# Optimization experiments

Measured on AMD Instinct MI355X. Metric: run time of the kernel, lower is better.

The kernel has to match this reference:

```python
import jax, jax.numpy as jnp
import numpy as np

NEG_SLOPE = 0.01  # torch nn.LeakyReLU default


def setup_inputs() -> dict:
    key = jax.random.key(0)
    k1, k2, k3, k4, k5 = jax.random.split(key, 5)
    B, C, N, O = 32, 512, 1024, 512
    x = jax.random.normal(k1, (B, C, N), dtype=jnp.float32)
    wq = jax.random.normal(k2, (C,), dtype=jnp.float32) * (1.0 / np.sqrt(C))
    wk = jax.random.normal(k3, (C,), dtype=jnp.float32) * (1.0 / np.sqrt(C))
    wm = jax.random.normal(k4, (O, C), dtype=jnp.float32) * (1.0 / np.sqrt(C))
    bm = jax.random.normal(k5, (O,), dtype=jnp.float32) * 0.01
    return {"x": x, "wq": wq, "wk": wk, "wm": wm, "bm": bm}


def reference(x, wq, wk, wm, bm):
    # x: [B, C, N]
    q = jnp.einsum('c,bcn->bn', wq, x)            # [B, N] (Conv1d C->1, k=1, no bias)
    k = jnp.einsum('c,bcn->bn', wk, x)            # [B, N]
    scores = q[:, None, :] + k[:, :, None]        # [B, N, N] additive broadcast
    scores = jnp.where(scores > 0, scores, NEG_SLOPE * scores)  # LeakyReLU
    att = jax.nn.softmax(scores, axis=-1)         # softmax over last dim
    agg = jnp.einsum('bcn,bmn->bcm', x, att)      # weighted aggregation [B, C, N]
    out = jnp.einsum('oc,bcm->bom', wm, agg) + bm[None, :, None]  # Conv1d k=1
    return jax.nn.relu(out)
```

## Files before the change

kernel.cpp:

```cpp
#include <hip/hip_runtime.h>


constexpr int B = 32, C = 512, N = 1024, O = 512;
constexpr float L2E = 1.4426950408889634f;

typedef _Float16 half8 __attribute__((ext_vector_type(8)));
typedef _Float16 half4v __attribute__((ext_vector_type(4)));
typedef _Float16 half2v __attribute__((ext_vector_type(2)));
typedef float f32x4 __attribute__((ext_vector_type(4)));

#if __has_builtin(__builtin_amdgcn_exp2f)
#define EXP2(x) __builtin_amdgcn_exp2f(x)
#else
#define EXP2(x) exp2f(x)
#endif

__device__ __forceinline__ half8 cvt8(float4 a, float4 b) {
  half8 h;
  h[0] = (_Float16)a.x; h[1] = (_Float16)a.y; h[2] = (_Float16)a.z; h[3] = (_Float16)a.w;
  h[4] = (_Float16)b.x; h[5] = (_Float16)b.y; h[6] = (_Float16)b.z; h[7] = (_Float16)b.w;
  return h;
}

__device__ __forceinline__ unsigned fenc(float x) {
  unsigned u = __float_as_uint(x);
  return (u & 0x80000000u) ? ~u : (u ^ 0x80000000u);
}
__device__ __forceinline__ float fdec(unsigned e) {
  unsigned u = (e & 0x80000000u) ? (e ^ 0x80000000u) : ~e;
  return __uint_as_float(u);
}

__global__ __launch_bounds__(256) void wmh_kernel(const float* __restrict__ wm,
                                                  _Float16* __restrict__ wmh,
                                                  unsigned* __restrict__ qmax_u) {
  int i = (blockIdx.x * 256 + threadIdx.x) * 8;
  float4 a = *(const float4*)(wm + i);
  float4 b = *(const float4*)(wm + i + 4);
  *(half8*)(wmh + i) = cvt8(a, b);
  if (blockIdx.x == 0 && threadIdx.x < 64) qmax_u[threadIdx.x] = 0u;
}

__global__ __launch_bounds__(256) void gemm_y_kernel(const float* __restrict__ x,
    const _Float16* __restrict__ wmh, const float* __restrict__ wq,
    const float* __restrict__ wk, float* __restrict__ q, float* __restrict__ k,
    unsigned* __restrict__ qmax_u, _Float16* __restrict__ Yt) {
  __shared__ half2v Xs[16 * 130];
  __shared__ float mred[4];
  int b  = blockIdx.y;
  int n0 = blockIdx.x * 128;
  int o0 = blockIdx.z * 128;
  int t = threadIdx.x;
  int w = t >> 6, l = t & 63;
  int nw = w >> 1, ow = w & 1;
  int lm = l & 15, q8 = (l >> 4) * 8, q4 = (l >> 4) * 4;

  int cp = t >> 4, ng = t & 15;
  bool doqk = (blockIdx.z == 0);
  float aq[8] = {}, ak[8] = {};

  const _Float16* wb[4];
#pragma unroll
  for (int j = 0; j < 4; ++j)
    wb[j] = wmh + (size_t)(o0 + ow * 64 + j * 16 + lm) * C + q8;

  f32x4 acc[4][4] = {};
  for (int c0 = 0; c0 < C; c0 += 32) {
    const float* xr = x + ((size_t)b * C + c0 + 2 * cp) * N + n0 + ng * 8;
    float4 a0 = *(const float4*)(xr);
    float4 a1 = *(const float4*)(xr + 4);
    float4 b0 = *(const float4*)(xr + N);
    float4 b1 = *(const float4*)(xr + N + 4);
    half8 bf[4];
#pragma unroll
    for (int j = 0; j < 4; ++j) bf[j] = *(const half8*)(wb[j] + c0);

    if (doqk) {
      float2 wq2 = *(const float2*)&wq[c0 + 2 * cp];
      float2 wk2 = *(const float2*)&wk[c0 + 2 * cp];
      aq[0] = fmaf(wq2.x, a0.x, fmaf(wq2.y, b0.x, aq[0]));
      aq[1] = fmaf(wq2.x, a0.y, fmaf(wq2.y, b0.y, aq[1]));
      aq[2] = fmaf(wq2.x, a0.z, fmaf(wq2.y, b0.z, aq[2]));
      aq[3] = fmaf(wq2.x, a0.w, fmaf(wq2.y, b0.w, aq[3]));
      aq[4] = fmaf(wq2.x, a1.x, fmaf(wq2.y, b1.x, aq[4]));
      aq[5] = fmaf(wq2.x, a1.y, fmaf(wq2.y, b1.y, aq[5]));
      aq[6] = fmaf(wq2.x, a1.z, fmaf(wq2.y, b1.z, aq[6]));
      aq[7] = fmaf(wq2.x, a1.w, fmaf(wq2.y, b1.w, aq[7]));
      ak[0] = fmaf(wk2.x, a0.x, fmaf(wk2.y, b0.x, ak[0]));
      ak[1] = fmaf(wk2.x, a0.y, fmaf(wk2.y, b0.y, ak[1]));
      ak[2] = fmaf(wk2.x, a0.z, fmaf(wk2.y, b0.z, ak[2]));
      ak[3] = fmaf(wk2.x, a0.w, fmaf(wk2.y, b0.w, ak[3]));
      ak[4] = fmaf(wk2.x, a1.x, fmaf(wk2.y, b1.x, ak[4]));
      ak[5] = fmaf(wk2.x, a1.y, fmaf(wk2.y, b1.y, ak[5]));
      ak[6] = fmaf(wk2.x, a1.z, fmaf(wk2.y, b1.z, ak[6]));
      ak[7] = fmaf(wk2.x, a1.w, fmaf(wk2.y, b1.w, ak[7]));
    }

    __syncthreads();
    {
      half2v* xp = &Xs[cp * 130 + ng * 8];
      xp[0] = half2v{(_Float16)a0.x, (_Float16)b0.x};
      xp[1] = half2v{(_Float16)a0.y, (_Float16)b0.y};
      xp[2] = half2v{(_Float16)a0.z, (_Float16)b0.z};
      xp[3] = half2v{(_Float16)a0.w, (_Float16)b0.w};
      xp[4] = half2v{(_Float16)a1.x, (_Float16)b1.x};
      xp[5] = half2v{(_Float16)a1.y, (_Float16)b1.y};
      xp[6] = half2v{(_Float16)a1.z, (_Float16)b1.z};
      xp[7] = half2v{(_Float16)a1.w, (_Float16)b1.w};
    }
    __syncthreads();

    half8 af[4];
#pragma unroll
    for (int i = 0; i < 4; ++i) {
      int nrow = nw * 64 + i * 16 + lm;
#pragma unroll
      for (int jp = 0; jp < 4; ++jp) {
        half2v p = Xs[(q4 + jp) * 130 + nrow];
        af[i][2 * jp]     = p[0];
        af[i][2 * jp + 1] = p[1];
      }
    }
#pragma unroll
    for (int i = 0; i < 4; ++i)
#pragma unroll
      for (int j = 0; j < 4; ++j)
        acc[i][j] = __builtin_amdgcn_mfma_f32_16x16x32_f16(af[i], bf[j], acc[i][j], 0, 0, 0);
  }

#pragma unroll
  for (int i = 0; i < 4; ++i) {
    int n_b = n0 + nw * 64 + i * 16 + (l >> 4) * 4;
#pragma unroll
    for (int j = 0; j < 4; ++j) {
      int o_c = o0 + ow * 64 + j * 16 + lm;
      half4v h;
      h[0] = (_Float16)acc[i][j][0];
      h[1] = (_Float16)acc[i][j][1];
      h[2] = (_Float16)acc[i][j][2];
      h[3] = (_Float16)acc[i][j][3];
      *(half4v*)&Yt[((size_t)b * O + o_c) * N + n_b] = h;
    }
  }

  if (doqk) {
    float* red = (float*)Xs;
    float qv_final = -1e30f;
    __syncthreads();
#pragma unroll
    for (int j = 0; j < 8; ++j) red[cp * 130 + ng * 8 + j] = aq[j];
    __syncthreads();
    if (t < 128) {
      float s = 0.f;
#pragma unroll
      for (int p = 0; p < 16; ++p) s += red[p * 130 + t];
      qv_final = L2E * s;
      q[b * N + n0 + t] = qv_final;
    }
    __syncthreads();
#pragma unroll
    for (int j = 0; j < 8; ++j) red[cp * 130 + ng * 8 + j] = ak[j];
    __syncthreads();
    if (t < 128) {
      float s = 0.f;
#pragma unroll
      for (int p = 0; p < 16; ++p) s += red[p * 130 + t];
      k[b * N + n0 + t] = L2E * s;
    }
    float m = qv_final;
#pragma unroll
    for (int off = 32; off > 0; off >>= 1) m = fmaxf(m, __shfl_down(m, off, 64));
    if ((t & 63) == 0) mred[t >> 6] = m;
    __syncthreads();
    if (t == 0) {
      float bmax = fmaxf(fmaxf(mred[0], mred[1]), fmaxf(mred[2], mred[3]));
      atomicMax(&qmax_u[b], fenc(bmax));
    }
  }
}

__global__ __launch_bounds__(512) void gemm_out_kernel(const _Float16* __restrict__ Yt,
    const float* __restrict__ q, const float* __restrict__ k,
    const unsigned* __restrict__ qmax_u, const float* __restrict__ bm,
    float* __restrict__ out) {
  __shared__ __align__(16) float qs[N];
  __shared__ __align__(16) _Float16 Ys[256 * 40];
  __shared__ float izs[128];
  int b  = blockIdx.y;
  int o0 = blockIdx.x * 256;
  int m0 = blockIdx.z * 128;
  int t = threadIdx.x;
  int w = t >> 6, l = t & 63;
  int lm = l & 15, g = l >> 4, q8 = g * 8;

  *(float2*)&qs[t * 2] = *(const float2*)&q[b * N + t * 2];

  float qmv = fdec(qmax_u[b]);
  float km = k[b * N + m0 + w * 16 + lm];
  float s0 = qmv + km;
  float M  = fmaxf(s0, 0.01f * s0);
  float k2 = km - M;
  float k3 = fmaf(0.01f, km, -M);

  half8 ones;
#pragma unroll
  for (int jj = 0; jj < 8; ++jj) ones[jj] = (_Float16)1.0f;
  f32x4 acc_z = {};
  int yr = t >> 1, yp = t & 1;
  const _Float16* ysrc = Yt + ((size_t)b * O + o0 + yr) * N + yp * 16;
  __syncthreads();

  f32x4 acc[16] = {};
  for (int n0k = 0; n0k < N; n0k += 32) {
    half8 y0 = *(const half8*)(ysrc + n0k);
    half8 y1 = *(const half8*)(ysrc + n0k + 8);
    float4 qa = *(const float4*)&qs[n0k + q8];
    float4 qb = *(const float4*)&qs[n0k + q8 + 4];
    float qv[8] = {qa.x, qa.y, qa.z, qa.w, qb.x, qb.y, qb.z, qb.w};
    half8 af;
#pragma unroll
    for (int jj = 0; jj < 8; ++jj) {
      float arg = fmaxf(qv[jj] + k2, fmaf(0.01f, qv[jj], k3));
      af[jj] = (_Float16)EXP2(arg);
    }
    acc_z = __builtin_amdgcn_mfma_f32_16x16x32_f16(af, ones, acc_z, 0, 0, 0);

    __syncthreads();
    *(half8*)&Ys[yr * 40 + yp * 16]     = y0;
    *(half8*)&Ys[yr * 40 + yp * 16 + 8] = y1;
    __syncthreads();

#pragma unroll
    for (int j = 0; j < 16; ++j) {
      half8 bf = *(const half8*)&Ys[(j * 16 + lm) * 40 + q8];
      acc[j] = __builtin_amdgcn_mfma_f32_16x16x32_f16(af, bf, acc[j], 0, 0, 0);
    }
  }

  if (lm == 0) {
#pragma unroll
    for (int r = 0; r < 4; ++r)
      izs[w * 16 + g * 4 + r] = 1.0f / acc_z[r];
  }
  __syncthreads();

  float4 iz4 = *(const float4*)&izs[w * 16 + g * 4];
#pragma unroll
  for (int j = 0; j < 16; ++j) {
    int o_c = o0 + j * 16 + lm;
    float bias = bm[o_c];
    int m_b = m0 + w * 16 + g * 4;
    float4 r;
    r.x = fmaxf(fmaf(acc[j][0], iz4.x, bias), 0.f);
    r.y = fmaxf(fmaf(acc[j][1], iz4.y, bias), 0.f);
    r.z = fmaxf(fmaf(acc[j][2], iz4.z, bias), 0.f);
    r.w = fmaxf(fmaf(acc[j][3], iz4.w, bias), 0.f);
    *(float4*)&out[((size_t)b * O + o_c) * N + m_b] = r;
  }
}

extern "C" void kernel_launch(void* const* d_in, const int* in_sizes, int n_in,
                              void* d_out, int out_size, void* d_ws, size_t ws_size,
                              hipStream_t stream) {
  const float* x  = (const float*)d_in[0];
  const float* wq = (const float*)d_in[1];
  const float* wk = (const float*)d_in[2];
  const float* wm = (const float*)d_in[3];
  const float* bm = (const float*)d_in[4];
  float* out = (float*)d_out;

  float* q    = (float*)d_ws;
  float* k    = q + B * N;
  unsigned* qmax_u = (unsigned*)(k + B * N);
  _Float16* wmh = (_Float16*)(qmax_u + 64);
  _Float16* Yt  = wmh + (size_t)O * C;

  wmh_kernel<<<dim3(O * C / (256 * 8)), 256, 0, stream>>>(wm, wmh, qmax_u);
  gemm_y_kernel<<<dim3(N / 128, B, O / 128), 256, 0, stream>>>(x, wmh, wq, wk, q, k, qmax_u, Yt);
  gemm_out_kernel<<<dim3(O / 256, B, N / 128), 512, 0, stream>>>(Yt, q, k, qmax_u, bm, out);
}
```

Baseline: 210.4 us.

## Double-buffer LDS in both GEMMs and switch output GEMM to 32x32 MFMA tiles

Both GEMM kernels now keep two LDS buffers and prefetch the next K-chunk from global memory into registers while MFMAs run on the current buffer, so each loop step needs one barrier instead of two. The output GEMM moves from 16x16x32 to 32x32x16 MFMA and doubles the m-tile per block to 256, which halves the grid and changes the accumulator layout and normalization indexing. The aim is to hide global load latency and to recompute the exp weights less often per Y element. The cost is more registers (8 f32x16 accumulators plus prefetch registers) and more LDS, which can lower occupancy.

```diff
diff --git a/kernel.cpp b/kernel.cpp
--- a/kernel.cpp
+++ b/kernel.cpp
@@ -8,6 +8,7 @@
 typedef _Float16 half4v __attribute__((ext_vector_type(4)));
 typedef _Float16 half2v __attribute__((ext_vector_type(2)));
 typedef float f32x4 __attribute__((ext_vector_type(4)));
+typedef float f32x16 __attribute__((ext_vector_type(16)));
 
 #if __has_builtin(__builtin_amdgcn_exp2f)
 #define EXP2(x) __builtin_amdgcn_exp2f(x)
@@ -45,7 +46,7 @@
     const _Float16* __restrict__ wmh, const float* __restrict__ wq,
     const float* __restrict__ wk, float* __restrict__ q, float* __restrict__ k,
     unsigned* __restrict__ qmax_u, _Float16* __restrict__ Yt) {
-  __shared__ half2v Xs[16 * 130];
+  __shared__ half2v Xs[2][16 * 130];
   __shared__ float mred[4];
   int b  = blockIdx.y;
   int n0 = blockIdx.x * 128;
@@ -63,62 +64,73 @@
 #pragma unroll
   for (int j = 0; j < 4; ++j)
     wb[j] = wmh + (size_t)(o0 + ow * 64 + j * 16 + lm) * C + q8;
+  const float* xbase = x + ((size_t)b * C + 2 * cp) * N + n0 + ng * 8;
+
+  float4 a0 = *(const float4*)(xbase);
+  float4 a1 = *(const float4*)(xbase + 4);
+  float4 b0 = *(const float4*)(xbase + N);
+  float4 b1 = *(const float4*)(xbase + N + 4);
+  half8 bf[4];
+#pragma unroll
+  for (int j = 0; j < 4; ++j) bf[j] = *(const half8*)(wb[j]);
+
+  if (doqk) {
+    float2 wq2 = *(const float2*)&wq[2 * cp];
+    float2 wk2 = *(const float2*)&wk[2 * cp];
+    aq[0] = fmaf(wq2.x, a0.x, fmaf(wq2.y, b0.x, aq[0]));
+    aq[1] = fmaf(wq2.x, a0.y, fmaf(wq2.y, b0.y, aq[1]));
+    aq[2] = fmaf(wq2.x, a0.z, fmaf(wq2.y, b0.z, aq[2]));
+    aq[3] = fmaf(wq2.x, a0.w, fmaf(wq2.y, b0.w, aq[3]));
+    aq[4] = fmaf(wq2.x, a1.x, fmaf(wq2.y, b1.x, aq[4]));
+    aq[5] = fmaf(wq2.x, a1.y, fmaf(wq2.y, b1.y, aq[5]));
+    aq[6] = fmaf(wq2.x, a1.z, fmaf(wq2.y, b1.z, aq[6]));
+    aq[7] = fmaf(wq2.x, a1.w, fmaf(wq2.y, b1.w, aq[7]));
+    ak[0] = fmaf(wk2.x, a0.x, fmaf(wk2.y, b0.x, ak[0]));
+    ak[1] = fmaf(wk2.x, a0.y, fmaf(wk2.y, b0.y, ak[1]));
+    ak[2] = fmaf(wk2.x, a0.z, fmaf(wk2.y, b0.z, ak[2]));
+    ak[3] = fmaf(wk2.x, a0.w, fmaf(wk2.y, b0.w, ak[3]));
+    ak[4] = fmaf(wk2.x, a1.x, fmaf(wk2.y, b1.x, ak[4]));
+    ak[5] = fmaf(wk2.x, a1.y, fmaf(wk2.y, b1.y, ak[5]));
+    ak[6] = fmaf(wk2.x, a1.z, fmaf(wk2.y, b1.z, ak[6]));
+    ak[7] = fmaf(wk2.x, a1.w, fmaf(wk2.y, b1.w, ak[7]));
+  }
+  {
+    half2v* xp = &Xs[0][cp * 130 + ng * 8];
+    xp[0] = half2v{(_Float16)a0.x, (_Float16)b0.x};
+    xp[1] = half2v{(_Float16)a0.y, (_Float16)b0.y};
+    xp[2] = half2v{(_Float16)a0.z, (_Float16)b0.z};
+    xp[3] = half2v{(_Float16)a0.w, (_Float16)b0.w};
+    xp[4] = half2v{(_Float16)a1.x, (_Float16)b1.x};
+    xp[5] = half2v{(_Float16)a1.y, (_Float16)b1.y};
+    xp[6] = half2v{(_Float16)a1.z, (_Float16)b1.z};
+    xp[7] = half2v{(_Float16)a1.w, (_Float16)b1.w};
+  }
+  __syncthreads();
 
   f32x4 acc[4][4] = {};
-  for (int c0 = 0; c0 < C; c0 += 32) {
-    const float* xr = x + ((size_t)b * C + c0 + 2 * cp) * N + n0 + ng * 8;
-    float4 a0 = *(const float4*)(xr);
-    float4 a1 = *(const float4*)(xr + 4);
-    float4 b0 = *(const float4*)(xr + N);
-    float4 b1 = *(const float4*)(xr + N + 4);
-    half8 bf[4];
-#pragma unroll
-    for (int j = 0; j < 4; ++j) bf[j] = *(const half8*)(wb[j] + c0);
-
-    if (doqk) {
-      float2 wq2 = *(const float2*)&wq[c0 + 2 * cp];
-      float2 wk2 = *(const float2*)&wk[c0 + 2 * cp];
-      aq[0] = fmaf(wq2.x, a0.x, fmaf(wq2.y, b0.x, aq[0]));
-      aq[1] = fmaf(wq2.x, a0.y, fmaf(wq2.y, b0.y, aq[1]));
-      aq[2] = fmaf(wq2.x, a0.z, fmaf(wq2.y, b0.z, aq[2]));
-      aq[3] = fmaf(wq2.x, a0.w, fmaf(wq2.y, b0.w, aq[3]));
-      aq[4] = fmaf(wq2.x, a1.x, fmaf(wq2.y, b1.x, aq[4]));
-      aq[5] = fmaf(wq2.x, a1.y, fmaf(wq2.y, b1.y, aq[5]));
-      aq[6] = fmaf(wq2.x, a1.z, fmaf(wq2.y, b1.z, aq[6]));
-      aq[7] = fmaf(wq2.x, a1.w, fmaf(wq2.y, b1.w, aq[7]));
-      ak[0] = fmaf(wk2.x, a0.x, fmaf(wk2.y, b0.x, ak[0]));
-      ak[1] = fmaf(wk2.x, a0.y, fmaf(wk2.y, b0.y, ak[1]));
-      ak[2] = fmaf(wk2.x, a0.z, fmaf(wk2.y, b0.z, ak[2]));
-      ak[3] = fmaf(wk2.x, a0.w, fmaf(wk2.y, b0.w, ak[3]));
-      ak[4] = fmaf(wk2.x, a1.x, fmaf(wk2.y, b1.x, ak[4]));
-      ak[5] = fmaf(wk2.x, a1.y, fmaf(wk2.y, b1.y, ak[5]));
-      ak[6] = fmaf(wk2.x, a1.z, fmaf(wk2.y, b1.z, ak[6]));
-      ak[7] = fmaf(wk2.x, a1.w, fmaf(wk2.y, b1.w, ak[7]));
-    }
-
-    __syncthreads();
-    {
-      half2v* xp = &Xs[cp * 130 + ng * 8];
-      xp[0] = half2v{(_Float16)a0.x, (_Float16)b0.x};
-      xp[1] = half2v{(_Float16)a0.y, (_Float16)b0.y};
-      xp[2] = half2v{(_Float16)a0.z, (_Float16)b0.z};
-      xp[3] = half2v{(_Float16)a0.w, (_Float16)b0.w};
-      xp[4] = half2v{(_Float16)a1.x, (_Float16)b1.x};
-      xp[5] = half2v{(_Float16)a1.y, (_Float16)b1.y};
-      xp[6] = half2v{(_Float16)a1.z, (_Float16)b1.z};
-      xp[7] = half2v{(_Float16)a1.w, (_Float16)b1.w};
-    }
-    __syncthreads();
-
+  for (int it = 0; it < 16; ++it) {
+    int p = it & 1;
+    float4 na0, na1, nb0, nb1;
+    half8 nbf[4];
+    if (it < 15) {
+      int c1 = (it + 1) * 32;
+      const float* xr = xbase + (size_t)c1 * N;
+      na0 = *(const float4*)(xr);
+      na1 = *(const float4*)(xr + 4);
+      nb0 = *(const float4*)(xr + N);
+      nb1 = *(const float4*)(xr + N + 4);
+#pragma unroll
+      for (int j = 0; j < 4; ++j) nbf[j] = *(const half8*)(wb[j] + c1);
+    }
     half8 af[4];
 #pragma unroll
     for (int i = 0; i < 4; ++i) {
       int nrow = nw * 64 + i * 16 + lm;
 #pragma unroll
       for (int jp = 0; jp < 4; ++jp) {
-        half2v p = Xs[(q4 + jp) * 130 + nrow];
-        af[i][2 * jp]     = p[0];
-        af[i][2 * jp + 1] = p[1];
+        half2v pr = Xs[p][(q4 + jp) * 130 + nrow];
+        af[i][2 * jp]     = pr[0];
+        af[i][2 * jp + 1] = pr[1];
       }
     }
 #pragma unroll
@@ -126,6 +138,42 @@
 #pragma unroll
       for (int j = 0; j < 4; ++j)
         acc[i][j] = __builtin_amdgcn_mfma_f32_16x16x32_f16(af[i], bf[j], acc[i][j], 0, 0, 0);
+
+    if (it < 15) {
+      int c1 = (it + 1) * 32;
+      if (doqk) {
+        float2 wq2 = *(const float2*)&wq[c1 + 2 * cp];
+        float2 wk2 = *(const float2*)&wk[c1 + 2 * cp];
+        aq[0] = fmaf(wq2.x, na0.x, fmaf(wq2.y, nb0.x, aq[0]));
+        aq[1] = fmaf(wq2.x, na0.y, fmaf(wq2.y, nb0.y, aq[1]));
+        aq[2] = fmaf(wq2.x, na0.z, fmaf(wq2.y, nb0.z, aq[2]));
+        aq[3] = fmaf(wq2.x, na0.w, fmaf(wq2.y, nb0.w, aq[3]));
+        aq[4] = fmaf(wq2.x, na1.x, fmaf(wq2.y, nb1.x, aq[4]));
+        aq[5] = fmaf(wq2.x, na1.y, fmaf(wq2.y, nb1.y, aq[5]));
+        aq[6] = fmaf(wq2.x, na1.z, fmaf(wq2.y, nb1.z, aq[6]));
+        aq[7] = fmaf(wq2.x, na1.w, fmaf(wq2.y, nb1.w, aq[7]));
+        ak[0] = fmaf(wk2.x, na0.x, fmaf(wk2.y, nb0.x, ak[0]));
+        ak[1] = fmaf(wk2.x, na0.y, fmaf(wk2.y, nb0.y, ak[1]));
+        ak[2] = fmaf(wk2.x, na0.z, fmaf(wk2.y, nb0.z, ak[2]));
+        ak[3] = fmaf(wk2.x, na0.w, fmaf(wk2.y, nb0.w, ak[3]));
+        ak[4] = fmaf(wk2.x, na1.x, fmaf(wk2.y, nb1.x, ak[4]));
+        ak[5] = fmaf(wk2.x, na1.y, fmaf(wk2.y, nb1.y, ak[5]));
+        ak[6] = fmaf(wk2.x, na1.z, fmaf(wk2.y, nb1.z, ak[6]));
+        ak[7] = fmaf(wk2.x, na1.w, fmaf(wk2.y, nb1.w, ak[7]));
+      }
+      half2v* xp = &Xs[p ^ 1][cp * 130 + ng * 8];
+      xp[0] = half2v{(_Float16)na0.x, (_Float16)nb0.x};
+      xp[1] = half2v{(_Float16)na0.y, (_Float16)nb0.y};
+      xp[2] = half2v{(_Float16)na0.z, (_Float16)nb0.z};
+      xp[3] = half2v{(_Float16)na0.w, (_Float16)nb0.w};
+      xp[4] = half2v{(_Float16)na1.x, (_Float16)nb1.x};
+      xp[5] = half2v{(_Float16)na1.y, (_Float16)nb1.y};
+      xp[6] = half2v{(_Float16)na1.z, (_Float16)nb1.z};
+      xp[7] = half2v{(_Float16)na1.w, (_Float16)nb1.w};
+#pragma unroll
+      for (int j = 0; j < 4; ++j) bf[j] = nbf[j];
+    }
+    __syncthreads();
   }
 
 #pragma unroll
@@ -184,78 +232,101 @@
     const unsigned* __restrict__ qmax_u, const float* __restrict__ bm,
     float* __restrict__ out) {
   __shared__ __align__(16) float qs[N];
-  __shared__ __align__(16) _Float16 Ys[256 * 40];
-  __shared__ float izs[128];
+  __shared__ __align__(16) _Float16 Ys[2][256 * 40];
+  __shared__ float izs[256];
   int b  = blockIdx.y;
   int o0 = blockIdx.x * 256;
-  int m0 = blockIdx.z * 128;
+  int m0 = blockIdx.z * 256;
   int t = threadIdx.x;
   int w = t >> 6, l = t & 63;
-  int lm = l & 15, g = l >> 4, q8 = g * 8;
+  int ml = l & 31, g2 = l >> 5;
 
   *(float2*)&qs[t * 2] = *(const float2*)&q[b * N + t * 2];
 
   float qmv = fdec(qmax_u[b]);
-  float km = k[b * N + m0 + w * 16 + lm];
+  float km = k[b * N + m0 + w * 32 + ml];
   float s0 = qmv + km;
   float M  = fmaxf(s0, 0.01f * s0);
-  float k2 = km - M;
-  float k3 = fmaf(0.01f, km, -M);
+  float kc2 = km - M;
+  float kc3 = fmaf(0.01f, km, -M);
 
   half8 ones;
 #pragma unroll
   for (int jj = 0; jj < 8; ++jj) ones[jj] = (_Float16)1.0f;
-  f32x4 acc_z = {};
+  f32x16 acc_z = {};
   int yr = t >> 1, yp = t & 1;
   const _Float16* ysrc = Yt + ((size_t)b * O + o0 + yr) * N + yp * 16;
+
+  {
+    half8 z0 = *(const half8*)(ysrc);
+    half8 z1 = *(const half8*)(ysrc + 8);
+    *(half8*)&Ys[0][yr * 40 + yp * 16]     = z0;
+    *(half8*)&Ys[0][yr * 40 + yp * 16 + 8] = z1;
+  }
   __syncthreads();
 
-  f32x4 acc[16] = {};
-  for (int n0k = 0; n0k < N; n0k += 32) {
-    half8 y0 = *(const half8*)(ysrc + n0k);
-    half8 y1 = *(const half8*)(ysrc + n0k + 8);
-    float4 qa = *(const float4*)&qs[n0k + q8];
-    float4 qb = *(const float4*)&qs[n0k + q8 + 4];
-    float qv[8] = {qa.x, qa.y, qa.z, qa.w, qb.x, qb.y, qb.z, qb.w};
-    half8 af;
-#pragma unroll
-    for (int jj = 0; jj < 8; ++jj) {
-      float arg = fmaxf(qv[jj] + k2, fmaf(0.01f, qv[jj], k3));
-      af[jj] = (_Float16)EXP2(arg);
-    }
-    acc_z = __builtin_amdgcn_mfma_f32_16x16x32_f16(af, ones, acc_z, 0, 0, 0);
-
-    __syncthreads();
-    *(half8*)&Ys[yr * 40 + yp * 16]     = y0;
-    *(half8*)&Ys[yr * 40 + yp * 16 + 8] = y1;
-    __syncthreads();
-
-#pragma unroll
-    for (int j = 0; j < 16; ++j) {
-      half8 bf = *(const half8*)&Ys[(j * 16 + lm) * 40 + q8];
-      acc[j] = __builtin_amdgcn_mfma_f32_16x16x32_f16(af, bf, acc[j], 0, 0, 0);
-    }
-  }
-
-  if (lm == 0) {
-#pragma unroll
-    for (int r = 0; r < 4; ++r)
-      izs[w * 16 + g * 4 + r] = 1.0f / acc_z[r];
+  f32x16 acc[8] = {};
+  for (int it = 0; it < N / 32; ++it) {
+    int p = it & 1;
+    int n0k = it * 32;
+    half8 z0, z1;
+    if (it < N / 32 - 1) {
+      z0 = *(const half8*)(ysrc + n0k + 32);
+      z1 = *(const half8*)(ysrc + n0k + 40);
+    }
+#pragma unroll
+    for (int kh = 0; kh < 2; ++kh) {
+      float4 qa = *(const float4*)&qs[n0k + kh * 16 + g2 * 8];
+      float4 qb = *(const float4*)&qs[n0k + kh * 16 + g2 * 8 + 4];
+      float qv[8] = {qa.x, qa.y, qa.z, qa.w, qb.x, qb.y, qb.z, qb.w};
+      half8 af;
+#pragma unroll
+      for (int jj = 0; jj < 8; ++jj) {
+        float arg = fmaxf(qv[jj] + kc2, fmaf(0.01f, qv[jj], kc3));
+        af[jj] = (_Float16)EXP2(arg);
+      }
+      acc_z = __builtin_amdgcn_mfma_f32_32x32x16_f16(af, ones, acc_z, 0, 0, 0);
+#pragma unroll
+      for (int s = 0; s < 8; ++s) {
+        half8 bf = *(const half8*)&Ys[p][(s * 32 + ml) * 40 + kh * 16 + g2 * 8];
+        acc[s] = __builtin_amdgcn_mfma_f32_32x32x16_f16(af, bf, acc[s], 0, 0, 0);
+      }
+    }
+    if (it < N / 32 - 1) {
+      *(half8*)&Ys[p ^ 1][yr * 40 + yp * 16]     = z0;
+      *(half8*)&Ys[p ^ 1][yr * 40 + yp * 16 + 8] = z1;
+    }
+    __syncthreads();
+  }
+
+  if (ml == 0) {
+#pragma unroll
+    for (int rq = 0; rq < 4; ++rq)
+#pragma unroll
+      for (int r = 0; r < 4; ++r)
+        izs[w * 32 + r + 8 * rq + 4 * g2] = 1.0f / acc_z[rq * 4 + r];
   }
   __syncthreads();
 
-  float4 iz4 = *(const float4*)&izs[w * 16 + g * 4];
-#pragma unroll
-  for (int j = 0; j < 16; ++j) {
-    int o_c = o0 + j * 16 + lm;
+  float4 izv[4];
+#pragma unroll
+  for (int rq = 0; rq < 4; ++rq)
+    izv[rq] = *(const float4*)&izs[w * 32 + 8 * rq + 4 * g2];
+
+#pragma unroll
+  for (int s = 0; s < 8; ++s) {
+    int o_c = o0 + s * 32 + ml;
     float bias = bm[o_c];
-    int m_b = m0 + w * 16 + g * 4;
-    float4 r;
-    r.x = fmaxf(fmaf(acc[j][0], iz4.x, bias), 0.f);
-    r.y = fmaxf(fmaf(acc[j][1], iz4.y, bias), 0.f);
-    r.z = fmaxf(fmaf(acc[j][2], iz4.z, bias), 0.f);
-    r.w = fmaxf(fmaf(acc[j][3], iz4.w, bias), 0.f);
-    *(float4*)&out[((size_t)b * O + o_c) * N + m_b] = r;
+#pragma unroll
+    for (int rq = 0; rq < 4; ++rq) {
+      int m_b = m0 + w * 32 + 8 * rq + 4 * g2;
+      float4 r;
+      r.x = fmaxf(fmaf(acc[s][rq * 4 + 0], izv[rq].x, bias), 0.f);
+      r.y = fmaxf(fmaf(acc[s][rq * 4 + 1], izv[rq].y, bias), 0.f);
+      r.z = fmaxf(fmaf(acc[s][rq * 4 + 2], izv[rq].z, bias), 0.f);
+      r.w = fmaxf(fmaf(acc[s][rq * 4 + 3], izv[rq].w, bias), 0.f);
+      *(float4*)&out[((size_t)b * O + o_c) * N + m_b] = r;
+    }
   }
 }
 
@@ -277,5 +348,5 @@
 
   wmh_kernel<<<dim3(O * C / (256 * 8)), 256, 0, stream>>>(wm, wmh, qmax_u);
   gemm_y_kernel<<<dim3(N / 128, B, O / 128), 256, 0, stream>>>(x, wmh, wq, wk, q, k, qmax_u, Yt);
-  gemm_out_kernel<<<dim3(O / 256, B, N / 128), 512, 0, stream>>>(Yt, q, k, qmax_u, bm, out);
-}
+  gemm_out_kernel<<<dim3(O / 256, B, N / 256), 512, 0, stream>>>(Yt, q, k, qmax_u, bm, out);
+}
```

After: 209.1 us. Within noise of the previous version (-0.6%).
